# Kernel tuning notes

Measured on AMD Instinct MI355X. Metric: run time of the kernel, lower is better.

Reference implementation:

```python
import jax, jax.numpy as jnp
import numpy as np

MUL = 64            # channel multiplicity per l
B = 8               # number of systems (equal-size MOLE segments)
N = 64000           # total edges
E = 8               # experts
OFFS = (0, 1, 4)    # per-l offsets inside D_total=9 rotation matrix
DTOT = 9
DIM = MUL * DTOT    # 1152

# ---- z-rotation scatter pattern (build_z_rot_multi): diag=cos(f*ang), antidiag=sin(f*ang), f = l - i ----
_rows, _anti, _freq = [], [], []
for l, off in zip(range(3), OFFS):
    for i in range(2 * l + 1):
        _rows.append(off + i); _anti.append(off + 2 * l - i); _freq.append(l - i)
_rows = np.array(_rows); _anti = np.array(_anti)
ROWS = jnp.array(_rows); FREQ = jnp.array(np.array(_freq, dtype=np.float32))
_nc = _rows != _anti  # exclude diag/antidiag overlap (center) from sin scatter
ROWS_NC = jnp.array(_rows[_nc]); ANTI_NC = jnp.array(_anti[_nc]); NCJ = jnp.array(np.where(_nc)[0])

# ---- per-m gather/scatter index tables (m_in_mask/m_out_mask) for irreps 64x0e+64x1o+64x2e ----
_c = np.arange(MUL)
M0_IDX = jnp.array(np.concatenate([_c, 64 + 3 * _c + 1, 256 + 5 * _c + 2]))                 # [192] centers
M1_IDX = jnp.array(np.stack([np.concatenate([64 + 3 * _c, 256 + 5 * _c + 1]),
                             np.concatenate([64 + 3 * _c + 2, 256 + 5 * _c + 3])], 1))      # [128,2] (-m,+m)
M2_IDX = jnp.array(np.stack([256 + 5 * _c, 256 + 5 * _c + 4], 1))                            # [64,2]


def _z_rot(angles):
    # scatter cos/sin into dense [N,9,9] block-diagonal z-rotation (irregular-access hot spot)
    c = jnp.cos(angles[:, None] * FREQ[None, :])
    s = jnp.sin(angles[:, None] * FREQ[None, :])
    X = jnp.zeros((angles.shape[0], DTOT, DTOT), angles.dtype)
    X = X.at[:, ROWS, ROWS].set(c)
    X = X.at[:, ROWS_NC, ANTI_NC].set(s[:, NCJ])
    return X


def _wigner(alpha, beta, gamma, Jf):
    Xa, Xb, Xc = _z_rot(alpha), _z_rot(beta), _z_rot(gamma)
    return Xa @ Jf @ Xb @ Jf @ Xc  # [N,9,9]


def _rotate(x, D):
    # apply block-diagonal Wigner D per l-block of each channel
    parts, col = [], 0
    for l, off in zip(range(3), OFFS):
        d = 2 * l + 1
        xl = x[:, col:col + MUL * d].reshape(-1, MUL, d)
        Dl = D[:, off:off + d, off:off + d]
        parts.append(jnp.einsum('nij,ncj->nci', Dl, xl).reshape(-1, MUL * d))
        col += MUL * d
    return jnp.concatenate(parts, axis=1)


def _mole(x, coef, We, Ws, be=None, bs=None):
    # MOLELinear: per-system expert-mixed weights + shared expert; equal-size segments
    W = jnp.einsum('be,eoi->boi', coef, We) + Ws[None]
    y = jnp.einsum('bti,boi->bto', x.reshape(B, -1, x.shape[-1]), W)
    if be is not None:
        y = y + (jnp.einsum('be,eo->bo', coef, be) + bs)[:, None, :]
    return y.reshape(x.shape[:-1] + (W.shape[1],))


def setup_inputs() -> dict:
    key = jax.random.key(0)
    ks = jax.random.split(key, 16)
    k0 = 1.0 / np.sqrt(192.0); k1 = 1.0 / np.sqrt(128.0 * 2.0); k2 = 1.0 / np.sqrt(64.0 * 2.0)
    two_pi = 6.2831853
    return dict(
        x=jax.random.normal(ks[0], (N, DIM), jnp.float32),
        alpha=jax.random.uniform(ks[1], (N,), jnp.float32, 0.0, two_pi),
        beta=jax.random.uniform(ks[2], (N,), jnp.float32, 0.0, two_pi),
        gamma=jax.random.uniform(ks[3], (N,), jnp.float32, 0.0, two_pi),
        coefficients=jax.nn.softmax(jax.random.normal(ks[4], (B, E), jnp.float32), axis=-1),
        Jd1=jax.random.normal(ks[5], (3, 3), jnp.float32),
        Jd2=jax.random.normal(ks[6], (5, 5), jnp.float32),
        w_m0=jax.random.normal(ks[7], (E, 192, 192), jnp.float32) * k0,
        b_m0=jax.random.normal(ks[8], (E, 192), jnp.float32) * k0,
        ws_m0=jax.random.normal(ks[9], (192, 192), jnp.float32) * k0,
        bs_m0=jax.random.normal(ks[10], (192,), jnp.float32) * k0,
        w_m1=jax.random.normal(ks[11], (E, 256, 128), jnp.float32) * k1,
        ws_m1=jax.random.normal(ks[12], (256, 128), jnp.float32) * k1,
        w_m2=jax.random.normal(ks[13], (E, 128, 64), jnp.float32) * k2,
        ws_m2=jax.random.normal(ks[14], (128, 64), jnp.float32) * k2,
    )


def reference(x, alpha, beta, gamma, coefficients, Jd1, Jd2,
              w_m0, b_m0, ws_m0, bs_m0, w_m1, ws_m1, w_m2, ws_m2):
    # block-diagonal J (Jd constants per l)
    Jf = (jnp.zeros((DTOT, DTOT), x.dtype)
          .at[0, 0].set(1.0)
          .at[1:4, 1:4].set(Jd1)
          .at[4:9, 4:9].set(Jd2))
    # rotate_in
    xr = _rotate(x, _wigner(alpha, beta, gamma, Jf))
    out = jnp.zeros((x.shape[0], DIM), x.dtype)
    # m = 0 path (MOLE linear with bias)
    out = out.at[:, M0_IDX].set(_mole(xr[:, M0_IDX], coefficients, w_m0, ws_m0, b_m0, bs_m0))
    # m > 0 paths (SO2_m_Linear, no bias)
    for IDX, We, Ws in ((M1_IDX, w_m1, ws_m1), (M2_IDX, w_m2, ws_m2)):
        C_out = We.shape[1] // 2
        xg = xr[:, IDX.reshape(-1)].reshape(-1, IDX.shape[0], 2).transpose(0, 2, 1)  # [N,2,C] rows=(-m,+m)
        y = _mole(xg, coefficients, We, Ws)                                            # [N,2,2*C_out]
        y_r, y_i = y[..., :C_out], y[..., C_out:]
        om = y_r[:, 0] - y_i[:, 1]
        op = y_r[:, 1] + y_i[:, 0]
        out = out.at[:, IDX.reshape(-1)].set(jnp.stack([om, op], -1).reshape(-1, 2 * C_out))
    # rotate_out (inverse rotation)
    out = _rotate(out, _wigner(-gamma, -beta, -alpha, Jf))
    return out
```

## Files before the change

kernel.cpp:

```cpp
#include <hip/hip_runtime.h>
#include <cstddef>

#define NS 64000
#define GROUP 8000
#define GPAD 8192

typedef __bf16 bf16x8 __attribute__((ext_vector_type(8)));
typedef float floatx4 __attribute__((ext_vector_type(4)));
typedef unsigned short ushort_t;

static const size_t BY_W0 = 0;
static const size_t BY_W1 = BY_W0 + 589824;
static const size_t BY_W2 = BY_W1 + 1048576;
static const size_t BY_B0 = BY_W2 + 262144;
static const size_t BY_X0 = BY_B0 + 6144;
static const size_t BY_X1 = BY_X0 + 25165824;
static const size_t BY_X2 = BY_X1 + 33554432;
static const size_t BY_Y0 = BY_X2 + 16777216;
static const size_t BY_Y1 = BY_Y0 + 50331648;
static const size_t BY_Y2 = BY_Y1 + 67108864;

__device__ __forceinline__ unsigned short f2bf(float f) {
    unsigned u = __float_as_uint(f);
    u += 0x7fff + ((u >> 16) & 1);
    return (unsigned short)(u >> 16);
}

__device__ __forceinline__ void async_cp16(const void* gsrc, void* ldst) {
    __builtin_amdgcn_global_load_lds(
        (const __attribute__((address_space(1))) unsigned int*)gsrc,
        (__attribute__((address_space(3))) unsigned int*)ldst, 16, 0, 0);
}

__device__ __forceinline__ size_t grow(int n) {
    int g = n / GROUP;
    return (size_t)g * GPAD + (size_t)(n - g * GROUP);
}

__global__ __launch_bounds__(256) void mix_kernel(
    const float* __restrict__ coef,
    const float* __restrict__ w_m0, const float* __restrict__ b_m0,
    const float* __restrict__ ws_m0, const float* __restrict__ bs_m0,
    const float* __restrict__ w_m1, const float* __restrict__ ws_m1,
    const float* __restrict__ w_m2, const float* __restrict__ ws_m2,
    ushort_t* __restrict__ W0, float* __restrict__ B0,
    ushort_t* __restrict__ W1, ushort_t* __restrict__ W2)
{
    int tid = blockIdx.x * 256 + threadIdx.x;
    if (tid < 294912) {
        int b = tid / 36864, rem = tid % 36864;
        float s = ws_m0[rem];
        #pragma unroll
        for (int e = 0; e < 8; e++) s += coef[b * 8 + e] * w_m0[e * 36864 + rem];
        W0[tid] = f2bf(s);
    } else if (tid < 296448) {
        int i2 = tid - 294912;
        int b = i2 / 192, o = i2 % 192;
        float s = bs_m0[o];
        #pragma unroll
        for (int e = 0; e < 8; e++) s += coef[b * 8 + e] * b_m0[e * 192 + o];
        B0[i2] = s;
    } else if (tid < 820736) {
        int i3 = tid - 296448;
        int b = i3 >> 16, rem = i3 & 65535;
        int o = rem >> 8, i = rem & 255;
        int r, cc; float sign = 1.0f;
        if (o < 128) { if (i < 128) { r = o;       cc = i; } else { r = 128 + o;      cc = i - 128; sign = -1.0f; } }
        else { int o2 = o - 128; if (i < 128) { r = 128 + o2; cc = i; } else { r = o2; cc = i - 128; } }
        int idx = r * 128 + cc;
        float s = ws_m1[idx];
        #pragma unroll
        for (int e = 0; e < 8; e++) s += coef[b * 8 + e] * w_m1[e * 32768 + idx];
        W1[i3] = f2bf(sign * s);
    } else if (tid < 951808) {
        int i4 = tid - 820736;
        int b = i4 >> 14, rem = i4 & 16383;
        int o = rem >> 7, i = rem & 127;
        int r, cc; float sign = 1.0f;
        if (o < 64) { if (i < 64) { r = o;      cc = i; } else { r = 64 + o;      cc = i - 64; sign = -1.0f; } }
        else { int o2 = o - 64; if (i < 64) { r = 64 + o2; cc = i; } else { r = o2; cc = i - 64; } }
        int idx = r * 64 + cc;
        float s = ws_m2[idx];
        #pragma unroll
        for (int e = 0; e < 8; e++) s += coef[b * 8 + e] * w_m2[e * 8192 + idx];
        W2[i4] = f2bf(sign * s);
    }
}

__device__ __forceinline__ void zrot1(float& v0, float& v2, float c, float s) {
    float t0 = c * v0 + s * v2;
    v2 = -s * v0 + c * v2;
    v0 = t0;
}
__device__ __forceinline__ void j1mul(const float* J, float& v0, float& v1, float& v2) {
    float w0 = J[0] * v0 + J[1] * v1 + J[2] * v2;
    float w1 = J[3] * v0 + J[4] * v1 + J[5] * v2;
    float w2 = J[6] * v0 + J[7] * v1 + J[8] * v2;
    v0 = w0; v1 = w1; v2 = w2;
}
__device__ __forceinline__ void zrot2(float& u0, float& u1, float& u3, float& u4,
                                      float c1, float s1, float c2, float s2) {
    float t0 = c2 * u0 + s2 * u4;
    u4 = -s2 * u0 + c2 * u4;
    u0 = t0;
    float t1 = c1 * u1 + s1 * u3;
    u3 = -s1 * u1 + c1 * u3;
    u1 = t1;
}
__device__ __forceinline__ void j2mul(const float* J, float& u0, float& u1, float& u2, float& u3, float& u4) {
    float w0 = J[0]  * u0 + J[1]  * u1 + J[2]  * u2 + J[3]  * u3 + J[4]  * u4;
    float w1 = J[5]  * u0 + J[6]  * u1 + J[7]  * u2 + J[8]  * u3 + J[9]  * u4;
    float w2 = J[10] * u0 + J[11] * u1 + J[12] * u2 + J[13] * u3 + J[14] * u4;
    float w3 = J[15] * u0 + J[16] * u1 + J[17] * u2 + J[18] * u3 + J[19] * u4;
    float w4 = J[20] * u0 + J[21] * u1 + J[22] * u2 + J[23] * u3 + J[24] * u4;
    u0 = w0; u1 = w1; u2 = w2; u3 = w3; u4 = w4;
}

__global__ __launch_bounds__(256) void rotate_fwd(
    const float* __restrict__ x,
    const float* __restrict__ alpha, const float* __restrict__ beta, const float* __restrict__ gamma_,
    const float* __restrict__ Jd1, const float* __restrict__ Jd2,
    ushort_t* __restrict__ X0, ushort_t* __restrict__ X1, ushort_t* __restrict__ X2)
{
    int t = threadIdx.x;
    int n = blockIdx.x * 4 + (t >> 6);
    int c = t & 63;
    const float* xr = x + (size_t)n * 576;
    float a = alpha[n], b = beta[n], g = gamma_[n];
    float sa, ca, sb, cb, sg, cg;
    __sincosf(a, &sa, &ca);
    __sincosf(b, &sb, &cb);
    __sincosf(g, &sg, &cg);
    float s2a = 2.f * sa * ca, c2a = ca * ca - sa * sa;
    float s2b = 2.f * sb * cb, c2b = cb * cb - sb * sb;
    float s2g = 2.f * sg * cg, c2g = cg * cg - sg * sg;

    float J1[9], J2[25];
    #pragma unroll
    for (int i = 0; i < 9; i++)  J1[i] = Jd1[i];
    #pragma unroll
    for (int i = 0; i < 25; i++) J2[i] = Jd2[i];

    float v0 = xr[64 + 3 * c], v1 = xr[64 + 3 * c + 1], v2 = xr[64 + 3 * c + 2];
    zrot1(v0, v2, cg, sg);
    j1mul(J1, v0, v1, v2);
    zrot1(v0, v2, cb, sb);
    j1mul(J1, v0, v1, v2);
    zrot1(v0, v2, ca, sa);

    float u0 = xr[256 + 5 * c], u1 = xr[256 + 5 * c + 1], u2 = xr[256 + 5 * c + 2],
          u3 = xr[256 + 5 * c + 3], u4 = xr[256 + 5 * c + 4];
    zrot2(u0, u1, u3, u4, cg, sg, c2g, s2g);
    j2mul(J2, u0, u1, u2, u3, u4);
    zrot2(u0, u1, u3, u4, cb, sb, c2b, s2b);
    j2mul(J2, u0, u1, u2, u3, u4);
    zrot2(u0, u1, u3, u4, ca, sa, c2a, s2a);

    size_t row = grow(n);
    size_t r0 = row * 192, r1 = row * 256, r2 = row * 128;
    X0[r0 + c]       = f2bf(xr[c]);
    X0[r0 + 64 + c]  = f2bf(v1);
    X0[r0 + 128 + c] = f2bf(u2);
    X1[r1 + c]       = f2bf(v0);
    X1[r1 + 64 + c]  = f2bf(u1);
    X1[r1 + 128 + c] = f2bf(v2);
    X1[r1 + 192 + c] = f2bf(u3);
    X2[r2 + c]       = f2bf(u0);
    X2[r2 + 64 + c]  = f2bf(u4);
}

template<int D, int BN, bool BIAS>
__global__ __launch_bounds__(256) void mfma_gemm(
    const ushort_t* __restrict__ X, const ushort_t* __restrict__ W,
    const float* __restrict__ bias, float* __restrict__ Y)
{
    constexpr int AG = 512;
    constexpr int BG = BN * 4;
    constexpr int TG = AG + BG;
    constexpr int NT = BN / 32;

    __shared__ ushort_t As[128 * 32];
    __shared__ ushort_t Bs[BN * 32];

    int t = threadIdx.x;
    int g = blockIdx.y >> 6;
    int tm = blockIdx.y & 63;
    int n0 = blockIdx.x * BN;

    const ushort_t* Xb = X + ((size_t)g * GPAD + (size_t)tm * 128) * D;
    const ushort_t* Wg = W + (size_t)g * D * D + (size_t)n0 * D;
    float* Yb = Y + ((size_t)g * GPAD + (size_t)tm * 128) * D + n0;

    int lane = t & 63;
    int w = t >> 6;
    int wm = w & 1, wn = w >> 1;
    int mi = lane & 15;
    int quad = lane >> 4;
    int qa = quad ^ ((mi >> 1) & 3);

    floatx4 acc[4][NT];
    #pragma unroll
    for (int i = 0; i < 4; i++)
        #pragma unroll
        for (int j = 0; j < NT; j++) acc[i][j] = (floatx4)0.f;

    #pragma unroll
    for (int k0 = 0; k0 < D; k0 += 32) {
        __syncthreads();
        #pragma unroll
        for (int it = 0; it < TG / 256; ++it) {
            int gi = it * 256 + t;
            if (gi < AG) {
                int row = gi >> 2;
                int q = (gi & 3) ^ ((row >> 1) & 3);
                async_cp16(Xb + (size_t)row * D + k0 + q * 8, &As[gi * 8]);
            } else {
                int gj = gi - AG;
                int row = gj >> 2;
                int q = (gj & 3) ^ ((row >> 1) & 3);
                async_cp16(Wg + (size_t)row * D + k0 + q * 8, &Bs[gj * 8]);
            }
        }
        __syncthreads();

        bf16x8 af[4], bfr[NT];
        #pragma unroll
        for (int i = 0; i < 4; i++) {
            int row = wm * 64 + i * 16 + mi;
            af[i] = *(const bf16x8*)&As[row * 32 + qa * 8];
        }
        #pragma unroll
        for (int j = 0; j < NT; j++) {
            int row = wn * (BN / 2) + j * 16 + mi;
            bfr[j] = *(const bf16x8*)&Bs[row * 32 + qa * 8];
        }
        #pragma unroll
        for (int i = 0; i < 4; i++)
            #pragma unroll
            for (int j = 0; j < NT; j++)
                acc[i][j] = __builtin_amdgcn_mfma_f32_16x16x32_bf16(af[i], bfr[j], acc[i][j], 0, 0, 0);
    }

    #pragma unroll
    for (int j = 0; j < NT; j++) {
        int col = wn * (BN / 2) + j * 16 + mi;
        float bv = 0.f;
        if (BIAS) bv = bias[g * D + n0 + col];
        #pragma unroll
        for (int i = 0; i < 4; i++) {
            int rbase = wm * 64 + i * 16 + quad * 4;
            #pragma unroll
            for (int r = 0; r < 4; r++) {
                Yb[(size_t)(rbase + r) * D + col] = acc[i][j][r] + bv;
            }
        }
    }
}

__global__ __launch_bounds__(256) void rotate_bwd(
    const float* __restrict__ Y0, const float* __restrict__ Y1, const float* __restrict__ Y2,
    const float* __restrict__ alpha, const float* __restrict__ beta, const float* __restrict__ gamma_,
    const float* __restrict__ Jd1, const float* __restrict__ Jd2,
    float* __restrict__ out)
{
    int t = threadIdx.x;
    int n = blockIdx.x * 4 + (t >> 6);
    int c = t & 63;
    float a = alpha[n], b = beta[n], g = gamma_[n];
    float sa, ca, sb, cb, sg, cg;
    __sincosf(a, &sa, &ca);
    __sincosf(b, &sb, &cb);
    __sincosf(g, &sg, &cg);
    sa = -sa; sb = -sb; sg = -sg;
    float s2a = 2.f * sa * ca, c2a = ca * ca - sa * sa;
    float s2b = 2.f * sb * cb, c2b = cb * cb - sb * sb;
    float s2g = 2.f * sg * cg, c2g = cg * cg - sg * sg;

    float J1[9], J2[25];
    #pragma unroll
    for (int i = 0; i < 9; i++)  J1[i] = Jd1[i];
    #pragma unroll
    for (int i = 0; i < 25; i++) J2[i] = Jd2[i];

    size_t row = grow(n);
    size_t r0 = row * 192, r1 = row * 256, r2 = row * 128;
    float* orow = out + (size_t)n * 576;

    orow[c] = Y0[r0 + c];

    float v0 = Y1[r1 + c], v1 = Y0[r0 + 64 + c], v2 = Y1[r1 + 128 + c];
    zrot1(v0, v2, ca, sa);
    j1mul(J1, v0, v1, v2);
    zrot1(v0, v2, cb, sb);
    j1mul(J1, v0, v1, v2);
    zrot1(v0, v2, cg, sg);
    orow[64 + 3 * c]     = v0;
    orow[64 + 3 * c + 1] = v1;
    orow[64 + 3 * c + 2] = v2;

    float u0 = Y2[r2 + c], u1 = Y1[r1 + 64 + c], u2 = Y0[r0 + 128 + c],
          u3 = Y1[r1 + 192 + c], u4 = Y2[r2 + 64 + c];
    zrot2(u0, u1, u3, u4, ca, sa, c2a, s2a);
    j2mul(J2, u0, u1, u2, u3, u4);
    zrot2(u0, u1, u3, u4, cb, sb, c2b, s2b);
    j2mul(J2, u0, u1, u2, u3, u4);
    zrot2(u0, u1, u3, u4, cg, sg, c2g, s2g);
    orow[256 + 5 * c]     = u0;
    orow[256 + 5 * c + 1] = u1;
    orow[256 + 5 * c + 2] = u2;
    orow[256 + 5 * c + 3] = u3;
    orow[256 + 5 * c + 4] = u4;
}

extern "C" void kernel_launch(void* const* d_in, const int* in_sizes, int n_in,
                              void* d_out, int out_size, void* d_ws, size_t ws_size,
                              hipStream_t stream)
{
    const float* x      = (const float*)d_in[0];
    const float* alpha  = (const float*)d_in[1];
    const float* beta   = (const float*)d_in[2];
    const float* gamma_ = (const float*)d_in[3];
    const float* coef   = (const float*)d_in[4];
    const float* Jd1    = (const float*)d_in[5];
    const float* Jd2    = (const float*)d_in[6];
    const float* w_m0   = (const float*)d_in[7];
    const float* b_m0   = (const float*)d_in[8];
    const float* ws_m0  = (const float*)d_in[9];
    const float* bs_m0  = (const float*)d_in[10];
    const float* w_m1   = (const float*)d_in[11];
    const float* ws_m1  = (const float*)d_in[12];
    const float* w_m2   = (const float*)d_in[13];
    const float* ws_m2  = (const float*)d_in[14];

    char* wsb = (char*)d_ws;
    ushort_t* W0 = (ushort_t*)(wsb + BY_W0);
    ushort_t* W1 = (ushort_t*)(wsb + BY_W1);
    ushort_t* W2 = (ushort_t*)(wsb + BY_W2);
    float*    B0 = (float*)(wsb + BY_B0);
    ushort_t* X0 = (ushort_t*)(wsb + BY_X0);
    ushort_t* X1 = (ushort_t*)(wsb + BY_X1);
    ushort_t* X2 = (ushort_t*)(wsb + BY_X2);
    float*    Y0 = (float*)(wsb + BY_Y0);
    float*    Y1 = (float*)(wsb + BY_Y1);
    float*    Y2 = (float*)(wsb + BY_Y2);
    float*    out = (float*)d_out;

    hipLaunchKernelGGL(mix_kernel, dim3(3718), dim3(256), 0, stream,
                       coef, w_m0, b_m0, ws_m0, bs_m0, w_m1, ws_m1, w_m2, ws_m2,
                       W0, B0, W1, W2);
    hipLaunchKernelGGL(rotate_fwd, dim3(NS / 4), dim3(256), 0, stream,
                       x, alpha, beta, gamma_, Jd1, Jd2, X0, X1, X2);
    hipLaunchKernelGGL((mfma_gemm<192, 64, true>),  dim3(3, 512), dim3(256), 0, stream, X0, W0, B0, Y0);
    hipLaunchKernelGGL((mfma_gemm<256, 128, false>), dim3(2, 512), dim3(256), 0, stream, X1, W1, (const float*)nullptr, Y1);
    hipLaunchKernelGGL((mfma_gemm<128, 128, false>), dim3(1, 512), dim3(256), 0, stream, X2, W2, (const float*)nullptr, Y2);
    hipLaunchKernelGGL(rotate_bwd, dim3(NS / 4), dim3(256), 0, stream,
                       Y0, Y1, Y2, alpha, beta, gamma_, Jd1, Jd2, out);
}
```

Before: 396.9 us.

## Fuse forward rotation, three MOLE GEMMs and inverse rotation into one kernel

Replaces the rotate_fwd, three GEMM and rotate_bwd kernels with one fused kernel per 64-edge tile. Rotated activations and GEMM outputs stay in XOR-swizzled LDS as bf16, and weights are read straight from global memory into registers. This removes the large bf16 X and fp32 Y intermediate buffers in global memory and several launches. In exchange the GEMM outputs are rounded to bf16, weights are re-read by each of the 1000 blocks without LDS staging, and the four waves carry unequal GEMM loads while holding large accumulator arrays.

```diff
diff --git a/kernel.cpp b/kernel.cpp
--- a/kernel.cpp
+++ b/kernel.cpp
@@ -3,7 +3,7 @@
 
 #define NS 64000
 #define GROUP 8000
-#define GPAD 8192
+#define TM 64
 
 typedef __bf16 bf16x8 __attribute__((ext_vector_type(8)));
 typedef float floatx4 __attribute__((ext_vector_type(4)));
@@ -13,28 +13,11 @@
 static const size_t BY_W1 = BY_W0 + 589824;
 static const size_t BY_W2 = BY_W1 + 1048576;
 static const size_t BY_B0 = BY_W2 + 262144;
-static const size_t BY_X0 = BY_B0 + 6144;
-static const size_t BY_X1 = BY_X0 + 25165824;
-static const size_t BY_X2 = BY_X1 + 33554432;
-static const size_t BY_Y0 = BY_X2 + 16777216;
-static const size_t BY_Y1 = BY_Y0 + 50331648;
-static const size_t BY_Y2 = BY_Y1 + 67108864;
 
 __device__ __forceinline__ unsigned short f2bf(float f) {
     unsigned u = __float_as_uint(f);
     u += 0x7fff + ((u >> 16) & 1);
     return (unsigned short)(u >> 16);
-}
-
-__device__ __forceinline__ void async_cp16(const void* gsrc, void* ldst) {
-    __builtin_amdgcn_global_load_lds(
-        (const __attribute__((address_space(1))) unsigned int*)gsrc,
-        (__attribute__((address_space(3))) unsigned int*)ldst, 16, 0, 0);
-}
-
-__device__ __forceinline__ size_t grow(int n) {
-    int g = n / GROUP;
-    return (size_t)g * GPAD + (size_t)(n - g * GROUP);
 }
 
 __global__ __launch_bounds__(256) void mix_kernel(
@@ -116,200 +99,219 @@
     u0 = w0; u1 = w1; u2 = w2; u3 = w3; u4 = w4;
 }
 
-__global__ __launch_bounds__(256) void rotate_fwd(
+__device__ __forceinline__ int sidx(int row, int k, int K) {
+    int gr = (k >> 3) ^ (row & 7);
+    return row * K + gr * 8 + (k & 7);
+}
+__device__ __forceinline__ float yread(const ushort_t* L, int row, int k, int K) {
+    unsigned u = L[sidx(row, k, K)];
+    return __uint_as_float(u << 16);
+}
+
+template<int K, int NT>
+__device__ __forceinline__ void gemm_seg(
+    floatx4 (*acc)[4],
+    const ushort_t* __restrict__ Wseg,
+    const ushort_t* XL_,
+    int mi, int quad)
+{
+    #pragma unroll
+    for (int k0 = 0; k0 < K; k0 += 32) {
+        bf16x8 af[4];
+        #pragma unroll
+        for (int ms = 0; ms < 4; ms++) {
+            int row = ms * 16 + mi;
+            int gr = ((k0 >> 3) + quad) ^ (row & 7);
+            af[ms] = *(const bf16x8*)&XL_[row * K + gr * 8];
+        }
+        bf16x8 bfr[NT];
+        #pragma unroll
+        for (int t = 0; t < NT; t++)
+            bfr[t] = *(const bf16x8*)&Wseg[(size_t)(t * 16 + mi) * K + k0 + quad * 8];
+        #pragma unroll
+        for (int t = 0; t < NT; t++)
+            #pragma unroll
+            for (int ms = 0; ms < 4; ms++)
+                acc[t][ms] = __builtin_amdgcn_mfma_f32_16x16x32_bf16(af[ms], bfr[t], acc[t][ms], 0, 0, 0);
+    }
+}
+
+template<int K, int NT, bool BIAS>
+__device__ __forceinline__ void ywrite(
+    floatx4 (*acc)[4], ushort_t* L, int n0, const float* __restrict__ bias,
+    int mi, int quad)
+{
+    #pragma unroll
+    for (int t = 0; t < NT; t++) {
+        int col = n0 + t * 16 + mi;
+        float bv = BIAS ? bias[col] : 0.f;
+        int gc = col >> 3, kw = col & 7;
+        #pragma unroll
+        for (int ms = 0; ms < 4; ms++) {
+            #pragma unroll
+            for (int r = 0; r < 4; r++) {
+                int m = ms * 16 + quad * 4 + r;
+                L[m * K + ((gc ^ (m & 7)) * 8) + kw] = f2bf(acc[t][ms][r] + bv);
+            }
+        }
+    }
+}
+
+__global__ __launch_bounds__(256, 2) void fused_kernel(
     const float* __restrict__ x,
     const float* __restrict__ alpha, const float* __restrict__ beta, const float* __restrict__ gamma_,
     const float* __restrict__ Jd1, const float* __restrict__ Jd2,
-    ushort_t* __restrict__ X0, ushort_t* __restrict__ X1, ushort_t* __restrict__ X2)
-{
+    const ushort_t* __restrict__ W0, const ushort_t* __restrict__ W1, const ushort_t* __restrict__ W2,
+    const float* __restrict__ B0,
+    float* __restrict__ out)
+{
+    __shared__ ushort_t XL[36864];
+    __shared__ float TR[64 * 6];
+    __shared__ float JL[34];
+
+    ushort_t* X0L = XL;
+    ushort_t* X1L = XL + 12288;
+    ushort_t* X2L = XL + 28672;
+
     int t = threadIdx.x;
-    int n = blockIdx.x * 4 + (t >> 6);
-    int c = t & 63;
-    const float* xr = x + (size_t)n * 576;
-    float a = alpha[n], b = beta[n], g = gamma_[n];
-    float sa, ca, sb, cb, sg, cg;
-    __sincosf(a, &sa, &ca);
-    __sincosf(b, &sb, &cb);
-    __sincosf(g, &sg, &cg);
-    float s2a = 2.f * sa * ca, c2a = ca * ca - sa * sa;
-    float s2b = 2.f * sb * cb, c2b = cb * cb - sb * sb;
-    float s2g = 2.f * sg * cg, c2g = cg * cg - sg * sg;
-
-    float J1[9], J2[25];
+    int w = t >> 6, lane = t & 63;
+    int g = blockIdx.x / 125;
+    int base = g * GROUP + (blockIdx.x % 125) * TM;
+
+    if (t < 64) {
+        int n = base + t;
+        float sa, ca, sb, cb, sg, cg;
+        __sincosf(alpha[n],  &sa, &ca);
+        __sincosf(beta[n],   &sb, &cb);
+        __sincosf(gamma_[n], &sg, &cg);
+        TR[t * 6 + 0] = sa; TR[t * 6 + 1] = ca;
+        TR[t * 6 + 2] = sb; TR[t * 6 + 3] = cb;
+        TR[t * 6 + 4] = sg; TR[t * 6 + 5] = cg;
+    } else if (t < 98) {
+        int j = t - 64;
+        JL[j] = (j < 9) ? Jd1[j] : Jd2[j - 9];
+    }
+    __syncthreads();
+
+    const float* J1 = JL;
+    const float* J2 = JL + 9;
+    int c = lane;
+
+    for (int i = 0; i < 16; i++) {
+        int nl = w * 16 + i;
+        const float* xr = x + (size_t)(base + nl) * 576;
+        float sa = TR[nl * 6 + 0], ca = TR[nl * 6 + 1];
+        float sb = TR[nl * 6 + 2], cb = TR[nl * 6 + 3];
+        float sg = TR[nl * 6 + 4], cg = TR[nl * 6 + 5];
+        float s2a = 2.f * sa * ca, c2a = ca * ca - sa * sa;
+        float s2b = 2.f * sb * cb, c2b = cb * cb - sb * sb;
+        float s2g = 2.f * sg * cg, c2g = cg * cg - sg * sg;
+
+        float v0 = xr[64 + 3 * c], v1 = xr[64 + 3 * c + 1], v2 = xr[64 + 3 * c + 2];
+        zrot1(v0, v2, cg, sg);
+        j1mul(J1, v0, v1, v2);
+        zrot1(v0, v2, cb, sb);
+        j1mul(J1, v0, v1, v2);
+        zrot1(v0, v2, ca, sa);
+
+        float u0 = xr[256 + 5 * c], u1 = xr[256 + 5 * c + 1], u2 = xr[256 + 5 * c + 2],
+              u3 = xr[256 + 5 * c + 3], u4 = xr[256 + 5 * c + 4];
+        zrot2(u0, u1, u3, u4, cg, sg, c2g, s2g);
+        j2mul(J2, u0, u1, u2, u3, u4);
+        zrot2(u0, u1, u3, u4, cb, sb, c2b, s2b);
+        j2mul(J2, u0, u1, u2, u3, u4);
+        zrot2(u0, u1, u3, u4, ca, sa, c2a, s2a);
+
+        X0L[sidx(nl, c, 192)]       = f2bf(xr[c]);
+        X0L[sidx(nl, 64 + c, 192)]  = f2bf(v1);
+        X0L[sidx(nl, 128 + c, 192)] = f2bf(u2);
+        X1L[sidx(nl, c, 256)]       = f2bf(v0);
+        X1L[sidx(nl, 64 + c, 256)]  = f2bf(u1);
+        X1L[sidx(nl, 128 + c, 256)] = f2bf(v2);
+        X1L[sidx(nl, 192 + c, 256)] = f2bf(u3);
+        X2L[sidx(nl, c, 128)]       = f2bf(u0);
+        X2L[sidx(nl, 64 + c, 128)]  = f2bf(u4);
+    }
+    __syncthreads();
+
+    int mi = lane & 15, quad = lane >> 4;
+    floatx4 acc[10][4];
     #pragma unroll
-    for (int i = 0; i < 9; i++)  J1[i] = Jd1[i];
-    #pragma unroll
-    for (int i = 0; i < 25; i++) J2[i] = Jd2[i];
-
-    float v0 = xr[64 + 3 * c], v1 = xr[64 + 3 * c + 1], v2 = xr[64 + 3 * c + 2];
-    zrot1(v0, v2, cg, sg);
-    j1mul(J1, v0, v1, v2);
-    zrot1(v0, v2, cb, sb);
-    j1mul(J1, v0, v1, v2);
-    zrot1(v0, v2, ca, sa);
-
-    float u0 = xr[256 + 5 * c], u1 = xr[256 + 5 * c + 1], u2 = xr[256 + 5 * c + 2],
-          u3 = xr[256 + 5 * c + 3], u4 = xr[256 + 5 * c + 4];
-    zrot2(u0, u1, u3, u4, cg, sg, c2g, s2g);
-    j2mul(J2, u0, u1, u2, u3, u4);
-    zrot2(u0, u1, u3, u4, cb, sb, c2b, s2b);
-    j2mul(J2, u0, u1, u2, u3, u4);
-    zrot2(u0, u1, u3, u4, ca, sa, c2a, s2a);
-
-    size_t row = grow(n);
-    size_t r0 = row * 192, r1 = row * 256, r2 = row * 128;
-    X0[r0 + c]       = f2bf(xr[c]);
-    X0[r0 + 64 + c]  = f2bf(v1);
-    X0[r0 + 128 + c] = f2bf(u2);
-    X1[r1 + c]       = f2bf(v0);
-    X1[r1 + 64 + c]  = f2bf(u1);
-    X1[r1 + 128 + c] = f2bf(v2);
-    X1[r1 + 192 + c] = f2bf(u3);
-    X2[r2 + c]       = f2bf(u0);
-    X2[r2 + 64 + c]  = f2bf(u4);
-}
-
-template<int D, int BN, bool BIAS>
-__global__ __launch_bounds__(256) void mfma_gemm(
-    const ushort_t* __restrict__ X, const ushort_t* __restrict__ W,
-    const float* __restrict__ bias, float* __restrict__ Y)
-{
-    constexpr int AG = 512;
-    constexpr int BG = BN * 4;
-    constexpr int TG = AG + BG;
-    constexpr int NT = BN / 32;
-
-    __shared__ ushort_t As[128 * 32];
-    __shared__ ushort_t Bs[BN * 32];
-
-    int t = threadIdx.x;
-    int g = blockIdx.y >> 6;
-    int tm = blockIdx.y & 63;
-    int n0 = blockIdx.x * BN;
-
-    const ushort_t* Xb = X + ((size_t)g * GPAD + (size_t)tm * 128) * D;
-    const ushort_t* Wg = W + (size_t)g * D * D + (size_t)n0 * D;
-    float* Yb = Y + ((size_t)g * GPAD + (size_t)tm * 128) * D + n0;
-
-    int lane = t & 63;
-    int w = t >> 6;
-    int wm = w & 1, wn = w >> 1;
-    int mi = lane & 15;
-    int quad = lane >> 4;
-    int qa = quad ^ ((mi >> 1) & 3);
-
-    floatx4 acc[4][NT];
-    #pragma unroll
-    for (int i = 0; i < 4; i++)
-        #pragma unroll
-        for (int j = 0; j < NT; j++) acc[i][j] = (floatx4)0.f;
-
-    #pragma unroll
-    for (int k0 = 0; k0 < D; k0 += 32) {
-        __syncthreads();
-        #pragma unroll
-        for (int it = 0; it < TG / 256; ++it) {
-            int gi = it * 256 + t;
-            if (gi < AG) {
-                int row = gi >> 2;
-                int q = (gi & 3) ^ ((row >> 1) & 3);
-                async_cp16(Xb + (size_t)row * D + k0 + q * 8, &As[gi * 8]);
-            } else {
-                int gj = gi - AG;
-                int row = gj >> 2;
-                int q = (gj & 3) ^ ((row >> 1) & 3);
-                async_cp16(Wg + (size_t)row * D + k0 + q * 8, &Bs[gj * 8]);
-            }
-        }
-        __syncthreads();
-
-        bf16x8 af[4], bfr[NT];
-        #pragma unroll
-        for (int i = 0; i < 4; i++) {
-            int row = wm * 64 + i * 16 + mi;
-            af[i] = *(const bf16x8*)&As[row * 32 + qa * 8];
-        }
-        #pragma unroll
-        for (int j = 0; j < NT; j++) {
-            int row = wn * (BN / 2) + j * 16 + mi;
-            bfr[j] = *(const bf16x8*)&Bs[row * 32 + qa * 8];
-        }
-        #pragma unroll
-        for (int i = 0; i < 4; i++)
-            #pragma unroll
-            for (int j = 0; j < NT; j++)
-                acc[i][j] = __builtin_amdgcn_mfma_f32_16x16x32_bf16(af[i], bfr[j], acc[i][j], 0, 0, 0);
-    }
-
-    #pragma unroll
-    for (int j = 0; j < NT; j++) {
-        int col = wn * (BN / 2) + j * 16 + mi;
-        float bv = 0.f;
-        if (BIAS) bv = bias[g * D + n0 + col];
-        #pragma unroll
-        for (int i = 0; i < 4; i++) {
-            int rbase = wm * 64 + i * 16 + quad * 4;
-            #pragma unroll
-            for (int r = 0; r < 4; r++) {
-                Yb[(size_t)(rbase + r) * D + col] = acc[i][j][r] + bv;
-            }
-        }
-    }
-}
-
-__global__ __launch_bounds__(256) void rotate_bwd(
-    const float* __restrict__ Y0, const float* __restrict__ Y1, const float* __restrict__ Y2,
-    const float* __restrict__ alpha, const float* __restrict__ beta, const float* __restrict__ gamma_,
-    const float* __restrict__ Jd1, const float* __restrict__ Jd2,
-    float* __restrict__ out)
-{
-    int t = threadIdx.x;
-    int n = blockIdx.x * 4 + (t >> 6);
-    int c = t & 63;
-    float a = alpha[n], b = beta[n], g = gamma_[n];
-    float sa, ca, sb, cb, sg, cg;
-    __sincosf(a, &sa, &ca);
-    __sincosf(b, &sb, &cb);
-    __sincosf(g, &sg, &cg);
-    sa = -sa; sb = -sb; sg = -sg;
-    float s2a = 2.f * sa * ca, c2a = ca * ca - sa * sa;
-    float s2b = 2.f * sb * cb, c2b = cb * cb - sb * sb;
-    float s2g = 2.f * sg * cg, c2g = cg * cg - sg * sg;
-
-    float J1[9], J2[25];
-    #pragma unroll
-    for (int i = 0; i < 9; i++)  J1[i] = Jd1[i];
-    #pragma unroll
-    for (int i = 0; i < 25; i++) J2[i] = Jd2[i];
-
-    size_t row = grow(n);
-    size_t r0 = row * 192, r1 = row * 256, r2 = row * 128;
-    float* orow = out + (size_t)n * 576;
-
-    orow[c] = Y0[r0 + c];
-
-    float v0 = Y1[r1 + c], v1 = Y0[r0 + 64 + c], v2 = Y1[r1 + 128 + c];
-    zrot1(v0, v2, ca, sa);
-    j1mul(J1, v0, v1, v2);
-    zrot1(v0, v2, cb, sb);
-    j1mul(J1, v0, v1, v2);
-    zrot1(v0, v2, cg, sg);
-    orow[64 + 3 * c]     = v0;
-    orow[64 + 3 * c + 1] = v1;
-    orow[64 + 3 * c + 2] = v2;
-
-    float u0 = Y2[r2 + c], u1 = Y1[r1 + 64 + c], u2 = Y0[r0 + 128 + c],
-          u3 = Y1[r1 + 192 + c], u4 = Y2[r2 + 64 + c];
-    zrot2(u0, u1, u3, u4, ca, sa, c2a, s2a);
-    j2mul(J2, u0, u1, u2, u3, u4);
-    zrot2(u0, u1, u3, u4, cb, sb, c2b, s2b);
-    j2mul(J2, u0, u1, u2, u3, u4);
-    zrot2(u0, u1, u3, u4, cg, sg, c2g, s2g);
-    orow[256 + 5 * c]     = u0;
-    orow[256 + 5 * c + 1] = u1;
-    orow[256 + 5 * c + 2] = u2;
-    orow[256 + 5 * c + 3] = u3;
-    orow[256 + 5 * c + 4] = u4;
+    for (int a = 0; a < 10; a++)
+        #pragma unroll
+        for (int b2 = 0; b2 < 4; b2++) acc[a][b2] = (floatx4)0.f;
+
+    const ushort_t* W0g = W0 + (size_t)g * 192 * 192;
+    const ushort_t* W1g = W1 + (size_t)g * 256 * 256;
+    const ushort_t* W2g = W2 + (size_t)g * 128 * 128;
+
+    if (w == 0) {
+        gemm_seg<192, 10>(acc, W0g, X0L, mi, quad);
+    } else if (w == 1) {
+        gemm_seg<256, 8>(acc, W1g, X1L, mi, quad);
+    } else if (w == 2) {
+        gemm_seg<256, 8>(acc, W1g + (size_t)128 * 256, X1L, mi, quad);
+    } else {
+        gemm_seg<192, 2>(acc, W0g + (size_t)160 * 192, X0L, mi, quad);
+        gemm_seg<128, 8>(acc + 2, W2g, X2L, mi, quad);
+    }
+
+    __syncthreads();
+
+    const float* B0g = B0 + g * 192;
+    if (w == 0) {
+        ywrite<192, 10, true>(acc, X0L, 0, B0g, mi, quad);
+    } else if (w == 1) {
+        ywrite<256, 8, false>(acc, X1L, 0, nullptr, mi, quad);
+    } else if (w == 2) {
+        ywrite<256, 8, false>(acc, X1L, 128, nullptr, mi, quad);
+    } else {
+        ywrite<192, 2, true>(acc, X0L, 160, B0g, mi, quad);
+        ywrite<128, 8, false>(acc + 2, X2L, 0, nullptr, mi, quad);
+    }
+    __syncthreads();
+
+    for (int i = 0; i < 16; i++) {
+        int nl = w * 16 + i;
+        float sa = -TR[nl * 6 + 0], ca = TR[nl * 6 + 1];
+        float sb = -TR[nl * 6 + 2], cb = TR[nl * 6 + 3];
+        float sg = -TR[nl * 6 + 4], cg = TR[nl * 6 + 5];
+        float s2a = 2.f * sa * ca, c2a = ca * ca - sa * sa;
+        float s2b = 2.f * sb * cb, c2b = cb * cb - sb * sb;
+        float s2g = 2.f * sg * cg, c2g = cg * cg - sg * sg;
+
+        float* orow = out + (size_t)(base + nl) * 576;
+
+        orow[c] = yread(X0L, nl, c, 192);
+
+        float v0 = yread(X1L, nl, c, 256);
+        float v1 = yread(X0L, nl, 64 + c, 192);
+        float v2 = yread(X1L, nl, 128 + c, 256);
+        zrot1(v0, v2, ca, sa);
+        j1mul(J1, v0, v1, v2);
+        zrot1(v0, v2, cb, sb);
+        j1mul(J1, v0, v1, v2);
+        zrot1(v0, v2, cg, sg);
+        orow[64 + 3 * c]     = v0;
+        orow[64 + 3 * c + 1] = v1;
+        orow[64 + 3 * c + 2] = v2;
+
+        float u0 = yread(X2L, nl, c, 128);
+        float u1 = yread(X1L, nl, 64 + c, 256);
+        float u2 = yread(X0L, nl, 128 + c, 192);
+        float u3 = yread(X1L, nl, 192 + c, 256);
+        float u4 = yread(X2L, nl, 64 + c, 128);
+        zrot2(u0, u1, u3, u4, ca, sa, c2a, s2a);
+        j2mul(J2, u0, u1, u2, u3, u4);
+        zrot2(u0, u1, u3, u4, cb, sb, c2b, s2b);
+        j2mul(J2, u0, u1, u2, u3, u4);
+        zrot2(u0, u1, u3, u4, cg, sg, c2g, s2g);
+        orow[256 + 5 * c]     = u0;
+        orow[256 + 5 * c + 1] = u1;
+        orow[256 + 5 * c + 2] = u2;
+        orow[256 + 5 * c + 3] = u3;
+        orow[256 + 5 * c + 4] = u4;
+    }
 }
 
 extern "C" void kernel_launch(void* const* d_in, const int* in_sizes, int n_in,
@@ -337,22 +339,11 @@
     ushort_t* W1 = (ushort_t*)(wsb + BY_W1);
     ushort_t* W2 = (ushort_t*)(wsb + BY_W2);
     float*    B0 = (float*)(wsb + BY_B0);
-    ushort_t* X0 = (ushort_t*)(wsb + BY_X0);
-    ushort_t* X1 = (ushort_t*)(wsb + BY_X1);
-    ushort_t* X2 = (ushort_t*)(wsb + BY_X2);
-    float*    Y0 = (float*)(wsb + BY_Y0);
-    float*    Y1 = (float*)(wsb + BY_Y1);
-    float*    Y2 = (float*)(wsb + BY_Y2);
     float*    out = (float*)d_out;
 
     hipLaunchKernelGGL(mix_kernel, dim3(3718), dim3(256), 0, stream,
                        coef, w_m0, b_m0, ws_m0, bs_m0, w_m1, ws_m1, w_m2, ws_m2,
                        W0, B0, W1, W2);
-    hipLaunchKernelGGL(rotate_fwd, dim3(NS / 4), dim3(256), 0, stream,
-                       x, alpha, beta, gamma_, Jd1, Jd2, X0, X1, X2);
-    hipLaunchKernelGGL((mfma_gemm<192, 64, true>),  dim3(3, 512), dim3(256), 0, stream, X0, W0, B0, Y0);
-    hipLaunchKernelGGL((mfma_gemm<256, 128, false>), dim3(2, 512), dim3(256), 0, stream, X1, W1, (const float*)nullptr, Y1);
-    hipLaunchKernelGGL((mfma_gemm<128, 128, false>), dim3(1, 512), dim3(256), 0, stream, X2, W2, (const float*)nullptr, Y2);
-    hipLaunchKernelGGL(rotate_bwd, dim3(NS / 4), dim3(256), 0, stream,
-                       Y0, Y1, Y2, alpha, beta, gamma_, Jd1, Jd2, out);
-}
+    hipLaunchKernelGGL(fused_kernel, dim3(1000), dim3(256), 0, stream,
+                       x, alpha, beta, gamma_, Jd1, Jd2, W0, W1, W2, B0, out);
+}
```

Result: faster. 337.9 us (-14.9%).
